# Kernel optimization log

Measured on AMD Instinct MI355X. Metric: run time of the kernel, lower is better.

The kernel has to match this reference:

```python
import jax, jax.numpy as jnp
import numpy as np

D_MODEL = 768
D_STATE = 16
EXPAND = 2
D_INNER = EXPAND * D_MODEL          # 1536
DT_RANK = D_MODEL // 16             # 48 (ceil(d_model/16))
D_CONV = 4
BATCH = 2
SEQ = 1024


def _init_params(key, prefix):
    ks = jax.random.split(key, 6)
    s = 0.02
    p = {}
    p[prefix + '_in_w'] = jax.random.normal(ks[0], (2 * D_INNER, D_MODEL), dtype=jnp.float32) * s
    p[prefix + '_conv_w'] = jax.random.normal(ks[1], (D_INNER, D_CONV), dtype=jnp.float32) * s
    p[prefix + '_conv_b'] = jnp.zeros((D_INNER,), dtype=jnp.float32)
    p[prefix + '_xproj_w'] = jax.random.normal(ks[2], (DT_RANK + 2 * D_STATE, D_INNER), dtype=jnp.float32) * s
    p[prefix + '_dt_w'] = jax.random.normal(ks[3], (D_INNER, DT_RANK), dtype=jnp.float32) * s
    p[prefix + '_dt_b'] = jax.random.normal(ks[4], (D_INNER,), dtype=jnp.float32) * s
    # S4D-real init: A = -[1..d_state] per channel, stored as log
    p[prefix + '_Alog'] = jnp.log(jnp.broadcast_to(jnp.arange(1, D_STATE + 1, dtype=jnp.float32), (D_INNER, D_STATE)))
    p[prefix + '_D'] = jnp.ones((D_INNER,), dtype=jnp.float32)
    p[prefix + '_out_w'] = jax.random.normal(ks[5], (D_MODEL, D_INNER), dtype=jnp.float32) * s
    return p


def setup_inputs() -> dict:
    key = jax.random.key(0)
    kx, kf, kb = jax.random.split(key, 3)
    inp = {'x': jax.random.normal(kx, (BATCH, SEQ, D_MODEL), dtype=jnp.float32)}
    inp.update(_init_params(kf, 'f'))
    inp.update(_init_params(kb, 'b'))
    return inp


def _mamba(x, in_w, conv_w, conv_b, xproj_w, dt_w, dt_b, Alog, Dskip, out_w):
    """One Mamba block (mamba_ssm semantics): in_proj -> causal depthwise conv ->
    SiLU -> (dt, B, C) projections -> selective scan -> SiLU(z) gate -> out_proj."""
    B, L, _ = x.shape
    xz = jnp.einsum('bld,ed->ble', x, in_w)            # (B, L, 2*d_inner)
    u, z = jnp.split(xz, 2, axis=-1)                    # each (B, L, d_inner)
    # causal depthwise conv1d, kernel D_CONV, left pad D_CONV-1
    u_t = u.transpose(0, 2, 1)                          # (B, d_inner, L)
    kern = conv_w[:, None, :]                           # (d_inner, 1, D_CONV)
    u_c = jax.lax.conv_general_dilated(u_t, kern, window_strides=(1,),
                                       padding=[(D_CONV - 1, 0)],
                                       feature_group_count=D_INNER)
    u = jax.nn.silu((u_c + conv_b[None, :, None]).transpose(0, 2, 1))  # (B, L, d_inner)
    x_dbl = jnp.einsum('bld,ed->ble', u, xproj_w)       # (B, L, dt_rank+2*d_state)
    dt, Bm, Cm = jnp.split(x_dbl, [DT_RANK, DT_RANK + D_STATE], axis=-1)
    delta = jax.nn.softplus(jnp.einsum('blr,dr->bld', dt, dt_w) + dt_b)  # (B, L, d_inner)
    A = -jnp.exp(Alog)                                  # (d_inner, d_state)
    dA = jnp.exp(jnp.einsum('bld,dn->bldn', delta, A))  # (B, L, d_inner, d_state)
    dBu = jnp.einsum('bld,bln,bld->bldn', delta, Bm, u) # (B, L, d_inner, d_state)

    def step(h, inp):
        dA_t, dBu_t, C_t = inp                           # (B,d,n),(B,d,n),(B,n)
        h = dA_t * h + dBu_t
        y = jnp.einsum('bdn,bn->bd', h, C_t)
        return h, y

    h0 = jnp.zeros((B, D_INNER, D_STATE), dtype=x.dtype)
    _, ys = jax.lax.scan(step, h0, (dA.transpose(1, 0, 2, 3),
                                    dBu.transpose(1, 0, 2, 3),
                                    Cm.transpose(1, 0, 2)))
    y = ys.transpose(1, 0, 2) + u * Dskip               # (B, L, d_inner)
    y = y * jax.nn.silu(z)
    return jnp.einsum('bld,od->blo', y, out_w)          # (B, L, d_model)


def reference(x, f_in_w, f_conv_w, f_conv_b, f_xproj_w, f_dt_w, f_dt_b, f_Alog, f_D, f_out_w,
              b_in_w, b_conv_w, b_conv_b, b_xproj_w, b_dt_w, b_dt_b, b_Alog, b_D, b_out_w):
    fwd = _mamba(x, f_in_w, f_conv_w, f_conv_b, f_xproj_w, f_dt_w, f_dt_b, f_Alog, f_D, f_out_w)
    bwd = jnp.flip(_mamba(jnp.flip(x, 1), b_in_w, b_conv_w, b_conv_b, b_xproj_w,
                          b_dt_w, b_dt_b, b_Alog, b_D, b_out_w), 1)
    return fwd + bwd  # merge == 'add'
```

## Files before the change

### kernel.cpp

```cpp
#include <hip/hip_runtime.h>

#define BATCH   2
#define SEQ     1024
#define DMODEL  768
#define DINNER  1536
#define DTRANK  48
#define DSTATE  16
#define NROWS   (BATCH*SEQ)
#define NCHUNK  64
#define LCHUNK  16

typedef unsigned short u16;
typedef __attribute__((ext_vector_type(8))) short short8;
typedef __attribute__((ext_vector_type(4))) float floatx4;

#define MFMA16(a,b,c) __builtin_amdgcn_mfma_f32_16x16x32_bf16(a,b,c,0,0,0)

__device__ __forceinline__ float us2f(u16 u) {
    union { unsigned int i; float f; } c; c.i = ((unsigned int)u) << 16; return c.f;
}
__device__ __forceinline__ u16 f2us(float f) {
    union { float f; unsigned int i; } c; c.f = f;
    unsigned int x = c.i;
    unsigned int lsb = (x >> 16) & 1u;
    x += 0x7fffu + lsb;
    return (u16)(x >> 16);
}
__device__ __forceinline__ float softplusf(float x) {
    return (x > 20.f) ? x : log1pf(__expf(x));
}

__device__ __forceinline__ void stage16(const void* g, void* l) {
    __builtin_amdgcn_global_load_lds((const __attribute__((address_space(1))) void*)g,
                                     (__attribute__((address_space(3))) void*)l, 16, 0, 0);
}

__global__ __launch_bounds__(256) void prep_all(
    const float* __restrict__ x,
    const float* __restrict__ fiw, const float* __restrict__ biw,
    const float* __restrict__ fxp, const float* __restrict__ bxp,
    const float* __restrict__ fow, const float* __restrict__ bow,
    const float* __restrict__ fdw, const float* __restrict__ bdw,
    u16* __restrict__ Xb, u16* __restrict__ Wf, u16* __restrict__ Wb,
    u16* __restrict__ XPhf, u16* __restrict__ XPlf,
    u16* __restrict__ XPhb, u16* __restrict__ XPlb,
    u16* __restrict__ Ocf, u16* __restrict__ Ocb,
    u16* __restrict__ DWh, u16* __restrict__ DWl)
{
    const int nx = NROWS * DMODEL;
    const int nw = 2 * DINNER * DMODEL;
    const int np = 128 * DINNER;
    const int no = DMODEL * DINNER;
    const int nd = DINNER * 64;
    int i = blockIdx.x * 256 + threadIdx.x;

    if (i < nx) { Xb[i] = f2us(x[i]); return; }
    i -= nx;
    if (i < nw) { Wf[i] = f2us(fiw[i]); return; }
    i -= nw;
    if (i < nw) { Wb[i] = f2us(biw[i]); return; }
    i -= nw;
    if (i < np) {
        const float f = (i < 80 * DINNER) ? fxp[i] : 0.f;
        const u16 h = f2us(f);
        XPhf[i] = h; XPlf[i] = f2us(f - us2f(h)); return;
    }
    i -= np;
    if (i < np) {
        const float f = (i < 80 * DINNER) ? bxp[i] : 0.f;
        const u16 h = f2us(f);
        XPhb[i] = h; XPlb[i] = f2us(f - us2f(h)); return;
    }
    i -= np;
    if (i < no) { Ocf[i] = f2us(fow[i]); return; }
    i -= no;
    if (i < no) { Ocb[i] = f2us(bow[i]); return; }
    i -= no;
    if (i < nd) {
        const int row = i >> 6, col = i & 63;
        const float f = (col < DTRANK) ? fdw[(size_t)row * DTRANK + col] : 0.f;
        const u16 h = f2us(f);
        DWh[i] = h; DWl[i] = f2us(f - us2f(h)); return;
    }
    i -= nd;
    if (i < nd) {
        const int row = i >> 6, col = i & 63;
        const float f = (col < DTRANK) ? bdw[(size_t)row * DTRANK + col] : 0.f;
        const u16 h = f2us(f);
        DWh[nd + i] = h; DWl[nd + i] = f2us(f - us2f(h));
    }
}

__global__ __launch_bounds__(256) void dprep2(
    const float* __restrict__ PS2,
    u16* __restrict__ XDh, u16* __restrict__ XDl,
    float* __restrict__ xdout)
{
    const int i = blockIdx.x * 256 + threadIdx.x;
    const int n1 = 2 * NROWS * 64;
    if (i < n1) {
        const int row = i >> 6, col = i & 63;
        float f = 0.f;
        if (col < DTRANK) {
            const int dir = row >> 11, r = row & 2047;
#pragma unroll
            for (int k = 0; k < 4; ++k)
                f += PS2[(((size_t)(dir * 4 + k) * NROWS) + r) * 80 + col];
        }
        const u16 h = f2us(f);
        XDh[i] = h;
        XDl[i] = f2us(f - us2f(h));
    } else {
        const int j = i - n1;
        const int row = j >> 5;
        const int col = 48 + (j & 31);
        const int dir = row >> 11, r = row & 2047;
        float f = 0.f;
#pragma unroll
        for (int k = 0; k < 4; ++k)
            f += PS2[(((size_t)(dir * 4 + k) * NROWS) + r) * 80 + col];
        xdout[(size_t)row * 80 + col] = f;
    }
}

__global__ __launch_bounds__(256) void gemm_delta(
    const u16* __restrict__ XDh, const u16* __restrict__ XDl,
    const u16* __restrict__ DWh, const u16* __restrict__ DWl,
    const float* __restrict__ fdtb, const float* __restrict__ bdtb,
    float* __restrict__ DLf, float* __restrict__ DLb)
{
    const int dir = blockIdx.z;
    const u16* ah = XDh + (size_t)dir * NROWS * 64;
    const u16* al = XDl + (size_t)dir * NROWS * 64;
    const u16* bh = DWh + (size_t)dir * DINNER * 64;
    const u16* bl = DWl + (size_t)dir * DINNER * 64;
    const float* bias = dir ? bdtb : fdtb;
    float* C = dir ? DLb : DLf;

    __shared__ __align__(16) u16 sAh[128 * 32];
    __shared__ __align__(16) u16 sAl[128 * 32];
    __shared__ __align__(16) u16 sBh[128 * 32];
    __shared__ __align__(16) u16 sBl[128 * 32];

    const int tid = threadIdx.x;
    const int lane = tid & 63;
    const int wave = tid >> 6;
    const int wm = wave >> 1, wn = wave & 1;
    const int m0 = blockIdx.y * 128, n0 = blockIdx.x * 128;
    const int lm = lane & 15, quad = lane >> 4;

    floatx4 acc[4][4];
#pragma unroll
    for (int i = 0; i < 4; ++i)
#pragma unroll
        for (int j = 0; j < 4; ++j)
            acc[i][j] = (floatx4){0.f, 0.f, 0.f, 0.f};

    for (int kt = 0; kt < 64; kt += 32) {
        __syncthreads();
#pragma unroll
        for (int c = 0; c < 2; ++c) {
            const int seg = wave * 2 + c;
            const int row = seg * 16 + (lane >> 2);
            const int col = kt + (lane & 3) * 8;
            stage16(ah + (size_t)(m0 + row) * 64 + col, (char*)sAh + seg * 1024);
            stage16(al + (size_t)(m0 + row) * 64 + col, (char*)sAl + seg * 1024);
            stage16(bh + (size_t)(n0 + row) * 64 + col, (char*)sBh + seg * 1024);
            stage16(bl + (size_t)(n0 + row) * 64 + col, (char*)sBl + seg * 1024);
        }
        __syncthreads();

        short8 afh[4], afl[4], bfh[4], bfl[4];
#pragma unroll
        for (int i = 0; i < 4; ++i) {
            const int ar = wm * 64 + i * 16 + lm;
            afh[i] = *reinterpret_cast<const short8*>(sAh + ar * 32 + quad * 8);
            afl[i] = *reinterpret_cast<const short8*>(sAl + ar * 32 + quad * 8);
            const int br = wn * 64 + i * 16 + lm;
            bfh[i] = *reinterpret_cast<const short8*>(sBh + br * 32 + quad * 8);
            bfl[i] = *reinterpret_cast<const short8*>(sBl + br * 32 + quad * 8);
        }
#pragma unroll
        for (int i = 0; i < 4; ++i)
#pragma unroll
            for (int j = 0; j < 4; ++j) {
                acc[i][j] = MFMA16(afh[i], bfh[j], acc[i][j]);
                acc[i][j] = MFMA16(afh[i], bfl[j], acc[i][j]);
                acc[i][j] = MFMA16(afl[i], bfh[j], acc[i][j]);
            }
    }

#pragma unroll
    for (int i = 0; i < 4; ++i)
#pragma unroll
        for (int j = 0; j < 4; ++j)
#pragma unroll
            for (int r = 0; r < 4; ++r) {
                const int row = m0 + wm * 64 + i * 16 + quad * 4 + r;
                const int col = n0 + wn * 64 + j * 16 + lm;
                C[(size_t)row * DINNER + col] = softplusf(acc[i][j][r] + bias[col]);
            }
}

__global__ __launch_bounds__(256) void gemm_mfma1(
    const u16* __restrict__ Ab,
    const u16* __restrict__ B0, const u16* __restrict__ B1,
    u16* __restrict__ U0, u16* __restrict__ Z0,
    u16* __restrict__ U1, u16* __restrict__ Z1)
{
    const u16* B = blockIdx.z ? B1 : B0;

    __shared__ __align__(16) u16 sA[128 * 32];
    __shared__ __align__(16) u16 sB[128 * 32];

    const int tid = threadIdx.x;
    const int lane = tid & 63;
    const int wave = tid >> 6;
    const int wm = wave >> 1, wn = wave & 1;
    const int m0 = blockIdx.y * 128, n0 = blockIdx.x * 128;
    const int lm = lane & 15, quad = lane >> 4;

    floatx4 acc[4][4];
#pragma unroll
    for (int i = 0; i < 4; ++i)
#pragma unroll
        for (int j = 0; j < 4; ++j)
            acc[i][j] = (floatx4){0.f, 0.f, 0.f, 0.f};

    for (int kt = 0; kt < DMODEL; kt += 32) {
        __syncthreads();
#pragma unroll
        for (int c = 0; c < 2; ++c) {
            const int seg = wave * 2 + c;
            const int row = seg * 16 + (lane >> 2);
            const int col = kt + (lane & 3) * 8;
            stage16(Ab + (size_t)(m0 + row) * DMODEL + col, (char*)sA + seg * 1024);
            stage16(B + (size_t)(n0 + row) * DMODEL + col, (char*)sB + seg * 1024);
        }
        __syncthreads();

        short8 af[4], bf[4];
#pragma unroll
        for (int i = 0; i < 4; ++i) {
            af[i] = *reinterpret_cast<const short8*>(sA + (wm * 64 + i * 16 + lm) * 32 + quad * 8);
            bf[i] = *reinterpret_cast<const short8*>(sB + (wn * 64 + i * 16 + lm) * 32 + quad * 8);
        }
#pragma unroll
        for (int i = 0; i < 4; ++i)
#pragma unroll
            for (int j = 0; j < 4; ++j)
                acc[i][j] = MFMA16(af[i], bf[j], acc[i][j]);
    }

    const bool isU = (n0 < DINNER);
    u16* dst = blockIdx.z ? (isU ? U1 : Z1) : (isU ? U0 : Z0);
    const int nb = isU ? n0 : n0 - DINNER;
#pragma unroll
    for (int i = 0; i < 4; ++i)
#pragma unroll
        for (int j = 0; j < 4; ++j)
#pragma unroll
            for (int r = 0; r < 4; ++r) {
                const int row = m0 + wm * 64 + i * 16 + quad * 4 + r;
                const int col = nb + wn * 64 + j * 16 + lm;
                dst[(size_t)row * DINNER + col] = f2us(acc[i][j][r]);
            }
}

__global__ __launch_bounds__(256) void gemm_xproj(
    const u16* __restrict__ A0, const u16* __restrict__ A1,
    const u16* __restrict__ Bh0, const u16* __restrict__ Bl0,
    const u16* __restrict__ Bh1, const u16* __restrict__ Bl1,
    float* __restrict__ PS2)
{
    const int dir = blockIdx.y >> 2, kseg = blockIdx.y & 3;
    const u16* A  = dir ? A1 : A0;
    const u16* Bh = dir ? Bh1 : Bh0;
    const u16* Bl = dir ? Bl1 : Bl0;
    float* out = PS2 + (size_t)blockIdx.y * NROWS * 80;

    __shared__ __align__(16) u16 sA[128 * 32];
    __shared__ __align__(16) u16 sBh[128 * 32];
    __shared__ __align__(16) u16 sBl[128 * 32];

    const int tid = threadIdx.x;
    const int lane = tid & 63;
    const int wave = tid >> 6;
    const int wm = wave >> 1, wn = wave & 1;
    const int m0 = blockIdx.x * 128;
    const int lm = lane & 15, quad = lane >> 4;

    floatx4 acc[4][4];
#pragma unroll
    for (int i = 0; i < 4; ++i)
#pragma unroll
        for (int j = 0; j < 4; ++j)
            acc[i][j] = (floatx4){0.f, 0.f, 0.f, 0.f};

    for (int kt = kseg * 384; kt < kseg * 384 + 384; kt += 32) {
        __syncthreads();
#pragma unroll
        for (int c = 0; c < 2; ++c) {
            const int seg = wave * 2 + c;
            const int row = seg * 16 + (lane >> 2);
            const int col = kt + (lane & 3) * 8;
            stage16(A + (size_t)(m0 + row) * DINNER + col, (char*)sA + seg * 1024);
            stage16(Bh + (size_t)row * DINNER + col, (char*)sBh + seg * 1024);
            stage16(Bl + (size_t)row * DINNER + col, (char*)sBl + seg * 1024);
        }
        __syncthreads();

        short8 af[4], bh[4], bl[4];
#pragma unroll
        for (int i = 0; i < 4; ++i) {
            af[i] = *reinterpret_cast<const short8*>(sA + (wm * 64 + i * 16 + lm) * 32 + quad * 8);
            bh[i] = *reinterpret_cast<const short8*>(sBh + (wn * 64 + i * 16 + lm) * 32 + quad * 8);
            bl[i] = *reinterpret_cast<const short8*>(sBl + (wn * 64 + i * 16 + lm) * 32 + quad * 8);
        }
#pragma unroll
        for (int i = 0; i < 4; ++i)
#pragma unroll
            for (int j = 0; j < 4; ++j) {
                acc[i][j] = MFMA16(af[i], bh[j], acc[i][j]);
                acc[i][j] = MFMA16(af[i], bl[j], acc[i][j]);
            }
    }

#pragma unroll
    for (int i = 0; i < 4; ++i)
#pragma unroll
        for (int j = 0; j < 4; ++j)
#pragma unroll
            for (int r = 0; r < 4; ++r) {
                const int row = m0 + wm * 64 + i * 16 + quad * 4 + r;
                const int col = wn * 64 + j * 16 + lm;
                if (col < 80)
                    out[(size_t)row * 80 + col] = acc[i][j][r];
            }
}

__global__ __launch_bounds__(256) void gemm_mfma_out(
    const u16* __restrict__ Y0, const u16* __restrict__ Y1,
    const u16* __restrict__ W0, const u16* __restrict__ W1,
    float* __restrict__ PS)
{
    const int dir = blockIdx.z >> 1, kseg = blockIdx.z & 1;
    const u16* A = dir ? Y1 : Y0;
    const u16* B = dir ? W1 : W0;
    float* out = PS + (size_t)blockIdx.z * NROWS * DMODEL;

    __shared__ __align__(16) u16 sA[128 * 32];
    __shared__ __align__(16) u16 sB[128 * 32];

    const int tid = threadIdx.x;
    const int lane = tid & 63;
    const int wave = tid >> 6;
    const int wm = wave >> 1, wn = wave & 1;
    const int m0 = blockIdx.y * 128, n0 = blockIdx.x * 128;
    const int lm = lane & 15, quad = lane >> 4;

    floatx4 acc[4][4];
#pragma unroll
    for (int i = 0; i < 4; ++i)
#pragma unroll
        for (int j = 0; j < 4; ++j)
            acc[i][j] = (floatx4){0.f, 0.f, 0.f, 0.f};

    for (int kt = kseg * 768; kt < kseg * 768 + 768; kt += 32) {
        __syncthreads();
#pragma unroll
        for (int c = 0; c < 2; ++c) {
            const int seg = wave * 2 + c;
            const int row = seg * 16 + (lane >> 2);
            const int col = kt + (lane & 3) * 8;
            stage16(A + (size_t)(m0 + row) * DINNER + col, (char*)sA + seg * 1024);
            stage16(B + (size_t)(n0 + row) * DINNER + col, (char*)sB + seg * 1024);
        }
        __syncthreads();

        short8 af[4], bf[4];
#pragma unroll
        for (int i = 0; i < 4; ++i) {
            af[i] = *reinterpret_cast<const short8*>(sA + (wm * 64 + i * 16 + lm) * 32 + quad * 8);
            bf[i] = *reinterpret_cast<const short8*>(sB + (wn * 64 + i * 16 + lm) * 32 + quad * 8);
        }
#pragma unroll
        for (int i = 0; i < 4; ++i)
#pragma unroll
            for (int j = 0; j < 4; ++j)
                acc[i][j] = MFMA16(af[i], bf[j], acc[i][j]);
    }

#pragma unroll
    for (int i = 0; i < 4; ++i)
#pragma unroll
        for (int j = 0; j < 4; ++j)
#pragma unroll
            for (int r = 0; r < 4; ++r) {
                const int row = m0 + wm * 64 + i * 16 + quad * 4 + r;
                const int col = n0 + wn * 64 + j * 16 + lm;
                out[(size_t)row * DMODEL + col] = acc[i][j][r];
            }
}

__global__ __launch_bounds__(256) void add4_kernel(
    const float* __restrict__ PS, float* __restrict__ out, int n4)
{
    const int i = blockIdx.x * 256 + threadIdx.x;
    if (i >= n4) return;
    const float4 a = reinterpret_cast<const float4*>(PS)[i];
    const float4 b = reinterpret_cast<const float4*>(PS + (size_t)NROWS * DMODEL)[i];
    const float4 c = reinterpret_cast<const float4*>(PS + (size_t)2 * NROWS * DMODEL)[i];
    const float4 d = reinterpret_cast<const float4*>(PS + (size_t)3 * NROWS * DMODEL)[i];
    reinterpret_cast<float4*>(out)[i] = make_float4(
        (a.x + b.x) + (c.x + d.x), (a.y + b.y) + (c.y + d.y),
        (a.z + b.z) + (c.z + d.z), (a.w + b.w) + (c.w + d.w));
}

__global__ __launch_bounds__(256) void conv_silu8(
    const u16* __restrict__ xuF, const u16* __restrict__ xuB,
    const float* __restrict__ wF, const float* __restrict__ wB,
    const float* __restrict__ bF, const float* __restrict__ bB,
    u16* __restrict__ ucF, u16* __restrict__ ucB)
{
    const int gid = blockIdx.x * 256 + threadIdx.x;
    const int dg = gid % 192;
    const int rest = gid / 192;
    const int bl = rest % NROWS;
    const int dir = rest / NROWS;
    const int b = bl / SEQ, l = bl % SEQ;
    const int d8 = dg * 8;

    const u16* xu   = dir ? xuB : xuF;
    const float* w  = dir ? wB : wF;
    const float* bs = dir ? bB : bF;
    u16* uc         = dir ? ucB : ucF;

    float acc[8];
    {
        const float4 b0 = *reinterpret_cast<const float4*>(bs + d8);
        const float4 b1 = *reinterpret_cast<const float4*>(bs + d8 + 4);
        acc[0]=b0.x; acc[1]=b0.y; acc[2]=b0.z; acc[3]=b0.w;
        acc[4]=b1.x; acc[5]=b1.y; acc[6]=b1.z; acc[7]=b1.w;
    }
    float wk[4][8];
#pragma unroll
    for (int dd = 0; dd < 8; ++dd) {
        const float4 wv = *reinterpret_cast<const float4*>(w + (size_t)(d8 + dd) * 4);
        wk[0][dd]=wv.x; wk[1][dd]=wv.y; wk[2][dd]=wv.z; wk[3][dd]=wv.w;
    }
#pragma unroll
    for (int k = 0; k < 4; ++k) {
        const int ls = (dir == 0) ? (l - 3 + k) : (l + 3 - k);
        if (ls >= 0 && ls < SEQ) {
            const short8 v = *reinterpret_cast<const short8*>(
                xu + ((size_t)b * SEQ + ls) * DINNER + d8);
#pragma unroll
            for (int dd = 0; dd < 8; ++dd)
                acc[dd] = fmaf(wk[k][dd], us2f((u16)v[dd]), acc[dd]);
        }
    }
    u16 out8[8];
#pragma unroll
    for (int dd = 0; dd < 8; ++dd) {
        const float s = acc[dd] * (1.f / (1.f + __expf(-acc[dd])));
        out8[dd] = f2us(s);
    }
    *reinterpret_cast<short8*>(uc + (size_t)bl * DINNER + d8) =
        *reinterpret_cast<const short8*>(out8);
}

__global__ __launch_bounds__(256) void scan_p1(
    const float* __restrict__ dF, const float* __restrict__ dB,
    const u16* __restrict__ ucF, const u16* __restrict__ ucB,
    const float* __restrict__ xdF, const float* __restrict__ xdB,
    float* __restrict__ SMh, float* __restrict__ esPool)
{
    const int bi = blockIdx.x;
    const int c = bi & (NCHUNK - 1);
    const int g = bi / NCHUNK;
    const int dg = g % 6;
    const int b  = (g / 6) & 1;
    const int dir = g / 12;
    const int tid = threadIdx.x;
    const int d = dg * 256 + tid;

    const float* delta = dir ? dB : dF;
    const u16*   uc    = dir ? ucB : ucF;
    const float* xdp   = dir ? xdB : xdF;

    float h[16];
#pragma unroll
    for (int n = 0; n < 16; ++n) h[n] = 0.f;
    float sumD = 0.f;

    for (int t = 0; t < LCHUNK; ++t) {
        const int tt = c * LCHUNK + t;
        const int l = dir ? (SEQ - 1 - tt) : tt;
        const size_t base = (size_t)b * SEQ + l;
        const float dlt = delta[base * DINNER + d];
        const float u   = us2f(uc[base * DINNER + d]);
        const float* xr = xdp + base * 80;
        const float4 B0 = *(const float4*)(xr + 48);
        const float4 B1 = *(const float4*)(xr + 52);
        const float4 B2 = *(const float4*)(xr + 56);
        const float4 B3 = *(const float4*)(xr + 60);
        const float Bv[16] = {B0.x, B0.y, B0.z, B0.w, B1.x, B1.y, B1.z, B1.w,
                              B2.x, B2.y, B2.z, B2.w, B3.x, B3.y, B3.z, B3.w};
        const float du = dlt * u;
        const float e = __expf(-dlt);
        float cur = e;
#pragma unroll
        for (int n = 0; n < 16; ++n) {
            h[n] = fmaf(cur, h[n], du * Bv[n]);
            cur *= e;
        }
        sumD += dlt;
    }
    float4* out = (float4*)(SMh + ((size_t)bi * 256 + tid) * 16);
    out[0] = make_float4(h[0], h[1], h[2], h[3]);
    out[1] = make_float4(h[4], h[5], h[6], h[7]);
    out[2] = make_float4(h[8], h[9], h[10], h[11]);
    out[3] = make_float4(h[12], h[13], h[14], h[15]);
    esPool[bi * 256 + tid] = __expf(-sumD);
}

__global__ __launch_bounds__(256) void scan_mid_par(
    float* __restrict__ SMh, const float* __restrict__ esPool)
{
    const int g = blockIdx.x >> 6;
    const int j = blockIdx.x & 63;
    const int tid = threadIdx.x;
    const int dd = tid >> 6;
    const int c  = tid & 63;
    const int d  = j * 4 + dd;
    const int slot = (g * NCHUNK + c) * 256 + d;

    float4* ph = (float4*)(SMh + (size_t)slot * 16);
    float h[16];
    {
        const float4 a = ph[0], b = ph[1], cc = ph[2], dv = ph[3];
        h[0]=a.x; h[1]=a.y; h[2]=a.z; h[3]=a.w;
        h[4]=b.x; h[5]=b.y; h[6]=b.z; h[7]=b.w;
        h[8]=cc.x; h[9]=cc.y; h[10]=cc.z; h[11]=cc.w;
        h[12]=dv.x; h[13]=dv.y; h[14]=dv.z; h[15]=dv.w;
    }
    float es = esPool[slot];

#pragma unroll
    for (int s = 1; s < NCHUNK; s <<= 1) {
        const float esB = es;
        const float es_p = __shfl_up(es, s, 64);
        float hp[16];
#pragma unroll
        for (int n = 0; n < 16; ++n) hp[n] = __shfl_up(h[n], s, 64);
        if (c >= s) {
            float cur = esB;
#pragma unroll
            for (int n = 0; n < 16; ++n) {
                h[n] = fmaf(cur, hp[n], h[n]);
                cur *= esB;
            }
            es = es_p * esB;
        }
    }
    float hx[16];
#pragma unroll
    for (int n = 0; n < 16; ++n) hx[n] = __shfl_up(h[n], 1, 64);
    if (c == 0) {
#pragma unroll
        for (int n = 0; n < 16; ++n) hx[n] = 0.f;
    }
    ph[0] = make_float4(hx[0], hx[1], hx[2], hx[3]);
    ph[1] = make_float4(hx[4], hx[5], hx[6], hx[7]);
    ph[2] = make_float4(hx[8], hx[9], hx[10], hx[11]);
    ph[3] = make_float4(hx[12], hx[13], hx[14], hx[15]);
}

__global__ __launch_bounds__(256) void scan_p2(
    const float* __restrict__ dF, const float* __restrict__ dB,
    const u16* __restrict__ ucF, const u16* __restrict__ ucB,
    const u16* __restrict__ zF, const u16* __restrict__ zB,
    const float* __restrict__ xdF, const float* __restrict__ xdB,
    const float* __restrict__ DF, const float* __restrict__ DB,
    const float* __restrict__ SMh,
    u16* __restrict__ yF, u16* __restrict__ yB)
{
    const int bi = blockIdx.x;
    const int c = bi & (NCHUNK - 1);
    const int g = bi / NCHUNK;
    const int dg = g % 6;
    const int b  = (g / 6) & 1;
    const int dir = g / 12;
    const int tid = threadIdx.x;
    const int d = dg * 256 + tid;

    const float* delta = dir ? dB : dF;
    const u16*   uc    = dir ? ucB : ucF;
    const u16*   zp    = dir ? zB : zF;
    const float* xdp   = dir ? xdB : xdF;
    u16*         y     = dir ? yB : yF;
    const float  Dd    = (dir ? DB : DF)[d];

    float h[16];
    {
        const float4* ph = (const float4*)(SMh + ((size_t)bi * 256 + tid) * 16);
        const float4 h0 = ph[0], h1 = ph[1], h2 = ph[2], h3 = ph[3];
        h[0]=h0.x; h[1]=h0.y; h[2]=h0.z; h[3]=h0.w;
        h[4]=h1.x; h[5]=h1.y; h[6]=h1.z; h[7]=h1.w;
        h[8]=h2.x; h[9]=h2.y; h[10]=h2.z; h[11]=h2.w;
        h[12]=h3.x; h[13]=h3.y; h[14]=h3.z; h[15]=h3.w;
    }

    for (int t = 0; t < LCHUNK; ++t) {
        const int tt = c * LCHUNK + t;
        const int l = dir ? (SEQ - 1 - tt) : tt;
        const size_t base = (size_t)b * SEQ + l;
        const float dlt = delta[base * DINNER + d];
        const float u   = us2f(uc[base * DINNER + d]);
        const float z   = us2f(zp[base * DINNER + d]);
        const float* xr = xdp + base * 80;
        const float4 B0 = *(const float4*)(xr + 48);
        const float4 B1 = *(const float4*)(xr + 52);
        const float4 B2 = *(const float4*)(xr + 56);
        const float4 B3 = *(const float4*)(xr + 60);
        const float4 C0 = *(const float4*)(xr + 64);
        const float4 C1 = *(const float4*)(xr + 68);
        const float4 C2 = *(const float4*)(xr + 72);
        const float4 C3 = *(const float4*)(xr + 76);
        const float Bv[16] = {B0.x, B0.y, B0.z, B0.w, B1.x, B1.y, B1.z, B1.w,
                              B2.x, B2.y, B2.z, B2.w, B3.x, B3.y, B3.z, B3.w};
        const float Cv[16] = {C0.x, C0.y, C0.z, C0.w, C1.x, C1.y, C1.z, C1.w,
                              C2.x, C2.y, C2.z, C2.w, C3.x, C3.y, C3.z, C3.w};
        const float du = dlt * u;
        const float e = __expf(-dlt);
        float cur = e;
        float yv = 0.f;
#pragma unroll
        for (int n = 0; n < 16; ++n) {
            h[n] = fmaf(cur, h[n], du * Bv[n]);
            yv = fmaf(h[n], Cv[n], yv);
            cur *= e;
        }
        yv += u * Dd;
        yv *= z * (1.f / (1.f + __expf(-z)));
        y[base * DINNER + d] = f2us(yv);
    }
}

extern "C" void kernel_launch(void* const* d_in, const int* in_sizes, int n_in,
                              void* d_out, int out_size, void* d_ws, size_t ws_size,
                              hipStream_t stream) {
    const float* x        = (const float*)d_in[0];
    const float* f_in_w   = (const float*)d_in[1];
    const float* f_conv_w = (const float*)d_in[2];
    const float* f_conv_b = (const float*)d_in[3];
    const float* f_xproj  = (const float*)d_in[4];
    const float* f_dt_w   = (const float*)d_in[5];
    const float* f_dt_b   = (const float*)d_in[6];
    const float* f_D      = (const float*)d_in[8];
    const float* f_out_w  = (const float*)d_in[9];
    const float* b_in_w   = (const float*)d_in[10];
    const float* b_conv_w = (const float*)d_in[11];
    const float* b_conv_b = (const float*)d_in[12];
    const float* b_xproj  = (const float*)d_in[13];
    const float* b_dt_w   = (const float*)d_in[14];
    const float* b_dt_b   = (const float*)d_in[15];
    const float* b_D      = (const float*)d_in[17];
    const float* b_out_w  = (const float*)d_in[18];

    char* ws = (char*)d_ws;
    size_t off = 0;
    auto carve = [&](size_t bytes) { char* p = ws + off; off += (bytes + 255) & ~(size_t)255; return p; };
    u16*   XU   = (u16*)  carve(2 * (size_t)NROWS * DINNER * 2);
    u16*   XZz  = (u16*)  carve(2 * (size_t)NROWS * DINNER * 2);
    u16*   UC   = (u16*)  carve(2 * (size_t)NROWS * DINNER * 2);
    u16*   Y    = (u16*)  carve(2 * (size_t)NROWS * DINNER * 2);
    float* XD   = (float*)carve(2 * (size_t)NROWS * 80 * 4);
    float* DL   = (float*)carve(2 * (size_t)NROWS * DINNER * 4);
    u16*   Xb   = (u16*)  carve((size_t)NROWS * DMODEL * 2);
    u16*   Wf   = (u16*)  carve(2 * (size_t)DINNER * DMODEL * 2);
    u16*   Wb   = (u16*)  carve(2 * (size_t)DINNER * DMODEL * 2);
    u16*   XPhf = (u16*)  carve(128 * (size_t)DINNER * 2);
    u16*   XPlf = (u16*)  carve(128 * (size_t)DINNER * 2);
    u16*   XPhb = (u16*)  carve(128 * (size_t)DINNER * 2);
    u16*   XPlb = (u16*)  carve(128 * (size_t)DINNER * 2);
    u16*   Ocf  = (u16*)  carve((size_t)DMODEL * DINNER * 2);
    u16*   Ocb  = (u16*)  carve((size_t)DMODEL * DINNER * 2);
    u16*   DWh  = (u16*)  carve(2 * (size_t)DINNER * 64 * 2);
    u16*   DWl  = (u16*)  carve(2 * (size_t)DINNER * 64 * 2);
    u16*   XDh  = (u16*)  carve(2 * (size_t)NROWS * 64 * 2);
    u16*   XDl  = (u16*)  carve(2 * (size_t)NROWS * 64 * 2);
    float* PS2  = (float*)carve(8 * (size_t)NROWS * 80 * 4);
    float* SMh  = (float*)carve((size_t)24 * NCHUNK * 256 * 16 * 4);
    float* esPool = (float*)carve((size_t)24 * NCHUNK * 256 * 4);
    float* PS   = (float*)carve(4 * (size_t)NROWS * DMODEL * 4);

    u16* XUb  = XU  + (size_t)NROWS * DINNER;
    u16* XZzb = XZz + (size_t)NROWS * DINNER;
    u16* UCb  = UC  + (size_t)NROWS * DINNER;
    u16* Yb   = Y   + (size_t)NROWS * DINNER;
    float* XDb = XD + (size_t)NROWS * 80;
    float* DLb = DL + (size_t)NROWS * DINNER;

    const dim3 blk(256);
    const int nprep = NROWS * DMODEL + 2 * (2 * DINNER * DMODEL) + 2 * (128 * DINNER)
                    + 2 * (DMODEL * DINNER) + 2 * (DINNER * 64);

    prep_all<<<dim3((nprep + 255) / 256), blk, 0, stream>>>(
        x, f_in_w, b_in_w, f_xproj, b_xproj, f_out_w, b_out_w, f_dt_w, b_dt_w,
        Xb, Wf, Wb, XPhf, XPlf, XPhb, XPlb, Ocf, Ocb, DWh, DWl);

    gemm_mfma1<<<dim3(2 * DINNER / 128, NROWS / 128, 2), blk, 0, stream>>>(
        Xb, Wf, Wb, XU, XZz, XUb, XZzb);

    conv_silu8<<<dim3(2 * NROWS * 192 / 256), blk, 0, stream>>>(
        XU, XUb, f_conv_w, b_conv_w, f_conv_b, b_conv_b, UC, UCb);

    gemm_xproj<<<dim3(NROWS / 128, 8), blk, 0, stream>>>(
        UC, UCb, XPhf, XPlf, XPhb, XPlb, PS2);

    dprep2<<<dim3((2 * NROWS * 64 + 2 * NROWS * 32) / 256), blk, 0, stream>>>(
        PS2, XDh, XDl, XD);

    gemm_delta<<<dim3(DINNER / 128, NROWS / 128, 2), blk, 0, stream>>>(
        XDh, XDl, DWh, DWl, f_dt_b, b_dt_b, DL, DLb);

    scan_p1<<<dim3(24 * NCHUNK), blk, 0, stream>>>(
        DL, DLb, UC, UCb, XD, XDb, SMh, esPool);

    scan_mid_par<<<dim3(24 * 64), blk, 0, stream>>>(SMh, esPool);

    scan_p2<<<dim3(24 * NCHUNK), blk, 0, stream>>>(
        DL, DLb, UC, UCb, XZz, XZzb, XD, XDb,
        f_D, b_D, SMh, Y, Yb);

    gemm_mfma_out<<<dim3(DMODEL / 128, NROWS / 128, 4), blk, 0, stream>>>(
        Y, Yb, Ocf, Ocb, PS);

    add4_kernel<<<dim3((NROWS * DMODEL / 4 + 255) / 256), blk, 0, stream>>>(
        PS, (float*)d_out, NROWS * DMODEL / 4);
}
```

Measured before the change: 314.4 us.

## Replace split-bf16 delta GEMM with fused fp32 VALU kernel and enlarge scan chunks

Removes the dprep2 split-precision conversion pass and the three-MFMA bf16 hi/lo delta GEMM. In their place, one fp32 VALU kernel reduces the partial x_proj sums into shared memory, keeps the 48 dt weights per channel in registers, and writes softplus(delta) directly. It also halves the number of scan chunks (chunk length 16 to 32) and adapts the chunk-prefix kernel to 32-wide shuffles. This saves a launch and intermediate traffic but puts the delta projection on scalar FMAs, and the longer chunks lengthen the sequential part of each scan pass.

```diff
diff --git a/kernel.cpp b/kernel.cpp
--- a/kernel.cpp
+++ b/kernel.cpp
@@ -7,8 +7,8 @@
 #define DTRANK  48
 #define DSTATE  16
 #define NROWS   (BATCH*SEQ)
-#define NCHUNK  64
-#define LCHUNK  16
+#define NCHUNK  32
+#define LCHUNK  32
 
 typedef unsigned short u16;
 typedef __attribute__((ext_vector_type(8))) short short8;
@@ -45,13 +45,13 @@
     u16* __restrict__ XPhf, u16* __restrict__ XPlf,
     u16* __restrict__ XPhb, u16* __restrict__ XPlb,
     u16* __restrict__ Ocf, u16* __restrict__ Ocb,
-    u16* __restrict__ DWh, u16* __restrict__ DWl)
+    float* __restrict__ DWT)
 {
     const int nx = NROWS * DMODEL;
     const int nw = 2 * DINNER * DMODEL;
     const int np = 128 * DINNER;
     const int no = DMODEL * DINNER;
-    const int nd = DINNER * 64;
+    const int nt = 2 * DTRANK * DINNER;
     int i = blockIdx.x * 256 + threadIdx.x;
 
     if (i < nx) { Xb[i] = f2us(x[i]); return; }
@@ -76,130 +76,71 @@
     i -= no;
     if (i < no) { Ocb[i] = f2us(bow[i]); return; }
     i -= no;
-    if (i < nd) {
-        const int row = i >> 6, col = i & 63;
-        const float f = (col < DTRANK) ? fdw[(size_t)row * DTRANK + col] : 0.f;
-        const u16 h = f2us(f);
-        DWh[i] = h; DWl[i] = f2us(f - us2f(h)); return;
-    }
-    i -= nd;
-    if (i < nd) {
-        const int row = i >> 6, col = i & 63;
-        const float f = (col < DTRANK) ? bdw[(size_t)row * DTRANK + col] : 0.f;
-        const u16 h = f2us(f);
-        DWh[nd + i] = h; DWl[nd + i] = f2us(f - us2f(h));
-    }
-}
-
-__global__ __launch_bounds__(256) void dprep2(
-    const float* __restrict__ PS2,
-    u16* __restrict__ XDh, u16* __restrict__ XDl,
-    float* __restrict__ xdout)
-{
-    const int i = blockIdx.x * 256 + threadIdx.x;
-    const int n1 = 2 * NROWS * 64;
-    if (i < n1) {
-        const int row = i >> 6, col = i & 63;
+    if (i < nt) {
+        const int dir = i / (DTRANK * DINNER);
+        const int rem = i % (DTRANK * DINNER);
+        const int k = rem / DINNER, d = rem % DINNER;
+        const float* w = dir ? bdw : fdw;
+        DWT[i] = w[(size_t)d * DTRANK + k];
+    }
+}
+
+__global__ __launch_bounds__(256) void delta_valu(
+    const float* __restrict__ PS2, const float* __restrict__ DWT,
+    const float* __restrict__ fdtb, const float* __restrict__ bdtb,
+    float* __restrict__ xdout,
+    float* __restrict__ DLf, float* __restrict__ DLb)
+{
+    const int slab = blockIdx.x / 6;
+    const int dg   = blockIdx.x % 6;
+    const int r0   = slab * 64;
+    const int dir  = r0 >> 11;
+    const int tid  = threadIdx.x;
+    const int d    = dg * 256 + tid;
+
+    __shared__ float sxd[64][48];
+
+    for (int j = tid; j < 64 * 48; j += 256) {
+        const int rr = r0 + j / 48;
+        const int col = j % 48;
+        const int rl = rr & 2047;
         float f = 0.f;
-        if (col < DTRANK) {
-            const int dir = row >> 11, r = row & 2047;
+#pragma unroll
+        for (int k = 0; k < 4; ++k)
+            f += PS2[(((size_t)(dir * 4 + k) * NROWS) + rl) * 80 + col];
+        sxd[j / 48][col] = f;
+    }
+    if (dg == 0) {
+        for (int j = tid; j < 64 * 32; j += 256) {
+            const int rr = r0 + j / 32;
+            const int col = 48 + (j % 32);
+            const int rl = rr & 2047;
+            float f = 0.f;
 #pragma unroll
             for (int k = 0; k < 4; ++k)
-                f += PS2[(((size_t)(dir * 4 + k) * NROWS) + r) * 80 + col];
-        }
-        const u16 h = f2us(f);
-        XDh[i] = h;
-        XDl[i] = f2us(f - us2f(h));
-    } else {
-        const int j = i - n1;
-        const int row = j >> 5;
-        const int col = 48 + (j & 31);
-        const int dir = row >> 11, r = row & 2047;
-        float f = 0.f;
-#pragma unroll
-        for (int k = 0; k < 4; ++k)
-            f += PS2[(((size_t)(dir * 4 + k) * NROWS) + r) * 80 + col];
-        xdout[(size_t)row * 80 + col] = f;
-    }
-}
-
-__global__ __launch_bounds__(256) void gemm_delta(
-    const u16* __restrict__ XDh, const u16* __restrict__ XDl,
-    const u16* __restrict__ DWh, const u16* __restrict__ DWl,
-    const float* __restrict__ fdtb, const float* __restrict__ bdtb,
-    float* __restrict__ DLf, float* __restrict__ DLb)
-{
-    const int dir = blockIdx.z;
-    const u16* ah = XDh + (size_t)dir * NROWS * 64;
-    const u16* al = XDl + (size_t)dir * NROWS * 64;
-    const u16* bh = DWh + (size_t)dir * DINNER * 64;
-    const u16* bl = DWl + (size_t)dir * DINNER * 64;
-    const float* bias = dir ? bdtb : fdtb;
-    float* C = dir ? DLb : DLf;
-
-    __shared__ __align__(16) u16 sAh[128 * 32];
-    __shared__ __align__(16) u16 sAl[128 * 32];
-    __shared__ __align__(16) u16 sBh[128 * 32];
-    __shared__ __align__(16) u16 sBl[128 * 32];
-
-    const int tid = threadIdx.x;
-    const int lane = tid & 63;
-    const int wave = tid >> 6;
-    const int wm = wave >> 1, wn = wave & 1;
-    const int m0 = blockIdx.y * 128, n0 = blockIdx.x * 128;
-    const int lm = lane & 15, quad = lane >> 4;
-
-    floatx4 acc[4][4];
-#pragma unroll
-    for (int i = 0; i < 4; ++i)
-#pragma unroll
-        for (int j = 0; j < 4; ++j)
-            acc[i][j] = (floatx4){0.f, 0.f, 0.f, 0.f};
-
-    for (int kt = 0; kt < 64; kt += 32) {
-        __syncthreads();
-#pragma unroll
-        for (int c = 0; c < 2; ++c) {
-            const int seg = wave * 2 + c;
-            const int row = seg * 16 + (lane >> 2);
-            const int col = kt + (lane & 3) * 8;
-            stage16(ah + (size_t)(m0 + row) * 64 + col, (char*)sAh + seg * 1024);
-            stage16(al + (size_t)(m0 + row) * 64 + col, (char*)sAl + seg * 1024);
-            stage16(bh + (size_t)(n0 + row) * 64 + col, (char*)sBh + seg * 1024);
-            stage16(bl + (size_t)(n0 + row) * 64 + col, (char*)sBl + seg * 1024);
-        }
-        __syncthreads();
-
-        short8 afh[4], afl[4], bfh[4], bfl[4];
-#pragma unroll
-        for (int i = 0; i < 4; ++i) {
-            const int ar = wm * 64 + i * 16 + lm;
-            afh[i] = *reinterpret_cast<const short8*>(sAh + ar * 32 + quad * 8);
-            afl[i] = *reinterpret_cast<const short8*>(sAl + ar * 32 + quad * 8);
-            const int br = wn * 64 + i * 16 + lm;
-            bfh[i] = *reinterpret_cast<const short8*>(sBh + br * 32 + quad * 8);
-            bfl[i] = *reinterpret_cast<const short8*>(sBl + br * 32 + quad * 8);
-        }
-#pragma unroll
-        for (int i = 0; i < 4; ++i)
-#pragma unroll
-            for (int j = 0; j < 4; ++j) {
-                acc[i][j] = MFMA16(afh[i], bfh[j], acc[i][j]);
-                acc[i][j] = MFMA16(afh[i], bfl[j], acc[i][j]);
-                acc[i][j] = MFMA16(afl[i], bfh[j], acc[i][j]);
-            }
-    }
-
-#pragma unroll
-    for (int i = 0; i < 4; ++i)
-#pragma unroll
-        for (int j = 0; j < 4; ++j)
-#pragma unroll
-            for (int r = 0; r < 4; ++r) {
-                const int row = m0 + wm * 64 + i * 16 + quad * 4 + r;
-                const int col = n0 + wn * 64 + j * 16 + lm;
-                C[(size_t)row * DINNER + col] = softplusf(acc[i][j][r] + bias[col]);
-            }
+                f += PS2[(((size_t)(dir * 4 + k) * NROWS) + rl) * 80 + col];
+            xdout[(size_t)rr * 80 + col] = f;
+        }
+    }
+
+    float dw[48];
+    {
+        const float* wt = DWT + (size_t)dir * DTRANK * DINNER;
+#pragma unroll
+        for (int k = 0; k < 48; ++k) dw[k] = wt[(size_t)k * DINNER + d];
+    }
+    const float dtb = (dir ? bdtb : fdtb)[d];
+    float* DL = dir ? DLb : DLf;
+    __syncthreads();
+
+    for (int rr = 0; rr < 64; ++rr) {
+        float acc = dtb;
+#pragma unroll
+        for (int k = 0; k < 48; ++k)
+            acc = fmaf(sxd[rr][k], dw[k], acc);
+        const int rl = (r0 + rr) & 2047;
+        DL[(size_t)rl * DINNER + d] = softplusf(acc);
+    }
 }
 
 __global__ __launch_bounds__(256) void gemm_mfma1(
@@ -528,12 +469,12 @@
 __global__ __launch_bounds__(256) void scan_mid_par(
     float* __restrict__ SMh, const float* __restrict__ esPool)
 {
-    const int g = blockIdx.x >> 6;
-    const int j = blockIdx.x & 63;
+    const int g = blockIdx.x >> 5;
+    const int j = blockIdx.x & 31;
     const int tid = threadIdx.x;
-    const int dd = tid >> 6;
-    const int c  = tid & 63;
-    const int d  = j * 4 + dd;
+    const int dd = tid >> 5;
+    const int c  = tid & 31;
+    const int d  = j * 8 + dd;
     const int slot = (g * NCHUNK + c) * 256 + d;
 
     float4* ph = (float4*)(SMh + (size_t)slot * 16);
@@ -550,10 +491,10 @@
 #pragma unroll
     for (int s = 1; s < NCHUNK; s <<= 1) {
         const float esB = es;
-        const float es_p = __shfl_up(es, s, 64);
+        const float es_p = __shfl_up(es, s, 32);
         float hp[16];
 #pragma unroll
-        for (int n = 0; n < 16; ++n) hp[n] = __shfl_up(h[n], s, 64);
+        for (int n = 0; n < 16; ++n) hp[n] = __shfl_up(h[n], s, 32);
         if (c >= s) {
             float cur = esB;
 #pragma unroll
@@ -566,7 +507,7 @@
     }
     float hx[16];
 #pragma unroll
-    for (int n = 0; n < 16; ++n) hx[n] = __shfl_up(h[n], 1, 64);
+    for (int n = 0; n < 16; ++n) hx[n] = __shfl_up(h[n], 1, 32);
     if (c == 0) {
 #pragma unroll
         for (int n = 0; n < 16; ++n) hx[n] = 0.f;
@@ -687,10 +628,7 @@
     u16*   XPlb = (u16*)  carve(128 * (size_t)DINNER * 2);
     u16*   Ocf  = (u16*)  carve((size_t)DMODEL * DINNER * 2);
     u16*   Ocb  = (u16*)  carve((size_t)DMODEL * DINNER * 2);
-    u16*   DWh  = (u16*)  carve(2 * (size_t)DINNER * 64 * 2);
-    u16*   DWl  = (u16*)  carve(2 * (size_t)DINNER * 64 * 2);
-    u16*   XDh  = (u16*)  carve(2 * (size_t)NROWS * 64 * 2);
-    u16*   XDl  = (u16*)  carve(2 * (size_t)NROWS * 64 * 2);
+    float* DWT  = (float*)carve(2 * (size_t)DTRANK * DINNER * 4);
     float* PS2  = (float*)carve(8 * (size_t)NROWS * 80 * 4);
     float* SMh  = (float*)carve((size_t)24 * NCHUNK * 256 * 16 * 4);
     float* esPool = (float*)carve((size_t)24 * NCHUNK * 256 * 4);
@@ -705,11 +643,11 @@
 
     const dim3 blk(256);
     const int nprep = NROWS * DMODEL + 2 * (2 * DINNER * DMODEL) + 2 * (128 * DINNER)
-                    + 2 * (DMODEL * DINNER) + 2 * (DINNER * 64);
+                    + 2 * (DMODEL * DINNER) + 2 * (DTRANK * DINNER);
 
     prep_all<<<dim3((nprep + 255) / 256), blk, 0, stream>>>(
         x, f_in_w, b_in_w, f_xproj, b_xproj, f_out_w, b_out_w, f_dt_w, b_dt_w,
-        Xb, Wf, Wb, XPhf, XPlf, XPhb, XPlb, Ocf, Ocb, DWh, DWl);
+        Xb, Wf, Wb, XPhf, XPlf, XPhb, XPlb, Ocf, Ocb, DWT);
 
     gemm_mfma1<<<dim3(2 * DINNER / 128, NROWS / 128, 2), blk, 0, stream>>>(
         Xb, Wf, Wb, XU, XZz, XUb, XZzb);
@@ -720,16 +658,13 @@
     gemm_xproj<<<dim3(NROWS / 128, 8), blk, 0, stream>>>(
         UC, UCb, XPhf, XPlf, XPhb, XPlb, PS2);
 
-    dprep2<<<dim3((2 * NROWS * 64 + 2 * NROWS * 32) / 256), blk, 0, stream>>>(
-        PS2, XDh, XDl, XD);
-
-    gemm_delta<<<dim3(DINNER / 128, NROWS / 128, 2), blk, 0, stream>>>(
-        XDh, XDl, DWh, DWl, f_dt_b, b_dt_b, DL, DLb);
+    delta_valu<<<dim3(64 * 6), blk, 0, stream>>>(
+        PS2, DWT, f_dt_b, b_dt_b, XD, DL, DLb);
 
     scan_p1<<<dim3(24 * NCHUNK), blk, 0, stream>>>(
         DL, DLb, UC, UCb, XD, XDb, SMh, esPool);
 
-    scan_mid_par<<<dim3(24 * 64), blk, 0, stream>>>(SMh, esPool);
+    scan_mid_par<<<dim3(24 * 32), blk, 0, stream>>>(SMh, esPool);
 
     scan_p2<<<dim3(24 * NCHUNK), blk, 0, stream>>>(
         DL, DLb, UC, UCb, XZz, XZzb, XD, XDb,
```

Measured after the change: 317.8 us. Within noise of the previous version (+1.1%).

## Fuse three-phase chunked scan into one cooperative kernel with grid syncs

Applied to the files above, without the earlier changes.

Merges scan_p1, scan_mid_par and scan_p2 into a single cooperative kernel that uses grid.sync() between the chunk-local scan, the cross-chunk prefix combine and the output pass. The chunk count is halved to 32 chunks of 32 steps so that 768 blocks can be co-resident for a cooperative launch, and the mid-phase shuffle width is reduced to 32. The goal is to remove two kernel launches and their gaps. In exchange each block runs a longer serial recurrence, there is less parallelism, and the two grid barriers add cost.

```diff
diff --git a/kernel.cpp b/kernel.cpp
--- a/kernel.cpp
+++ b/kernel.cpp
@@ -1,4 +1,5 @@
 #include <hip/hip_runtime.h>
+#include <hip/hip_cooperative_groups.h>
 
 #define BATCH   2
 #define SEQ     1024
@@ -7,8 +8,8 @@
 #define DTRANK  48
 #define DSTATE  16
 #define NROWS   (BATCH*SEQ)
-#define NCHUNK  64
-#define LCHUNK  16
+#define NCHUNK  32
+#define LCHUNK  32
 
 typedef unsigned short u16;
 typedef __attribute__((ext_vector_type(8))) short short8;
@@ -470,12 +471,17 @@
         *reinterpret_cast<const short8*>(out8);
 }
 
-__global__ __launch_bounds__(256) void scan_p1(
+__global__ __launch_bounds__(256) void scan_fused(
     const float* __restrict__ dF, const float* __restrict__ dB,
     const u16* __restrict__ ucF, const u16* __restrict__ ucB,
+    const u16* __restrict__ zF, const u16* __restrict__ zB,
     const float* __restrict__ xdF, const float* __restrict__ xdB,
-    float* __restrict__ SMh, float* __restrict__ esPool)
-{
+    const float* __restrict__ DF, const float* __restrict__ DB,
+    float* __restrict__ SMh, float* __restrict__ esPool,
+    u16* __restrict__ yF, u16* __restrict__ yB)
+{
+    cooperative_groups::grid_group grid = cooperative_groups::this_grid();
+
     const int bi = blockIdx.x;
     const int c = bi & (NCHUNK - 1);
     const int g = bi / NCHUNK;
@@ -487,7 +493,10 @@
 
     const float* delta = dir ? dB : dF;
     const u16*   uc    = dir ? ucB : ucF;
+    const u16*   zp    = dir ? zB : zF;
     const float* xdp   = dir ? xdB : xdF;
+    u16*         y     = dir ? yB : yF;
+    const float  Dd    = (dir ? DB : DF)[d];
 
     float h[16];
 #pragma unroll
@@ -517,92 +526,68 @@
         }
         sumD += dlt;
     }
-    float4* out = (float4*)(SMh + ((size_t)bi * 256 + tid) * 16);
-    out[0] = make_float4(h[0], h[1], h[2], h[3]);
-    out[1] = make_float4(h[4], h[5], h[6], h[7]);
-    out[2] = make_float4(h[8], h[9], h[10], h[11]);
-    out[3] = make_float4(h[12], h[13], h[14], h[15]);
-    esPool[bi * 256 + tid] = __expf(-sumD);
-}
-
-__global__ __launch_bounds__(256) void scan_mid_par(
-    float* __restrict__ SMh, const float* __restrict__ esPool)
-{
-    const int g = blockIdx.x >> 6;
-    const int j = blockIdx.x & 63;
-    const int tid = threadIdx.x;
-    const int dd = tid >> 6;
-    const int c  = tid & 63;
-    const int d  = j * 4 + dd;
-    const int slot = (g * NCHUNK + c) * 256 + d;
-
-    float4* ph = (float4*)(SMh + (size_t)slot * 16);
-    float h[16];
     {
-        const float4 a = ph[0], b = ph[1], cc = ph[2], dv = ph[3];
-        h[0]=a.x; h[1]=a.y; h[2]=a.z; h[3]=a.w;
-        h[4]=b.x; h[5]=b.y; h[6]=b.z; h[7]=b.w;
-        h[8]=cc.x; h[9]=cc.y; h[10]=cc.z; h[11]=cc.w;
-        h[12]=dv.x; h[13]=dv.y; h[14]=dv.z; h[15]=dv.w;
-    }
-    float es = esPool[slot];
-
-#pragma unroll
-    for (int s = 1; s < NCHUNK; s <<= 1) {
-        const float esB = es;
-        const float es_p = __shfl_up(es, s, 64);
-        float hp[16];
-#pragma unroll
-        for (int n = 0; n < 16; ++n) hp[n] = __shfl_up(h[n], s, 64);
-        if (c >= s) {
-            float cur = esB;
-#pragma unroll
-            for (int n = 0; n < 16; ++n) {
-                h[n] = fmaf(cur, hp[n], h[n]);
-                cur *= esB;
+        float4* out = (float4*)(SMh + ((size_t)bi * 256 + tid) * 16);
+        out[0] = make_float4(h[0], h[1], h[2], h[3]);
+        out[1] = make_float4(h[4], h[5], h[6], h[7]);
+        out[2] = make_float4(h[8], h[9], h[10], h[11]);
+        out[3] = make_float4(h[12], h[13], h[14], h[15]);
+        esPool[bi * 256 + tid] = __expf(-sumD);
+    }
+
+    grid.sync();
+
+    {
+        const int g2 = blockIdx.x >> 5;
+        const int j  = blockIdx.x & 31;
+        const int dd = tid >> 5;
+        const int cc = tid & 31;
+        const int d2 = j * 8 + dd;
+        const int slot = (g2 * NCHUNK + cc) * 256 + d2;
+
+        float4* ph = (float4*)(SMh + (size_t)slot * 16);
+        float hh[16];
+        {
+            const float4 a = ph[0], bb = ph[1], c2 = ph[2], dv = ph[3];
+            hh[0]=a.x; hh[1]=a.y; hh[2]=a.z; hh[3]=a.w;
+            hh[4]=bb.x; hh[5]=bb.y; hh[6]=bb.z; hh[7]=bb.w;
+            hh[8]=c2.x; hh[9]=c2.y; hh[10]=c2.z; hh[11]=c2.w;
+            hh[12]=dv.x; hh[13]=dv.y; hh[14]=dv.z; hh[15]=dv.w;
+        }
+        float es = esPool[slot];
+
+#pragma unroll
+        for (int s = 1; s < NCHUNK; s <<= 1) {
+            const float esB = es;
+            const float es_p = __shfl_up(es, s, 32);
+            float hp[16];
+#pragma unroll
+            for (int n = 0; n < 16; ++n) hp[n] = __shfl_up(hh[n], s, 32);
+            if (cc >= s) {
+                float cur = esB;
+#pragma unroll
+                for (int n = 0; n < 16; ++n) {
+                    hh[n] = fmaf(cur, hp[n], hh[n]);
+                    cur *= esB;
+                }
+                es = es_p * esB;
             }
-            es = es_p * esB;
-        }
-    }
-    float hx[16];
-#pragma unroll
-    for (int n = 0; n < 16; ++n) hx[n] = __shfl_up(h[n], 1, 64);
-    if (c == 0) {
-#pragma unroll
-        for (int n = 0; n < 16; ++n) hx[n] = 0.f;
-    }
-    ph[0] = make_float4(hx[0], hx[1], hx[2], hx[3]);
-    ph[1] = make_float4(hx[4], hx[5], hx[6], hx[7]);
-    ph[2] = make_float4(hx[8], hx[9], hx[10], hx[11]);
-    ph[3] = make_float4(hx[12], hx[13], hx[14], hx[15]);
-}
-
-__global__ __launch_bounds__(256) void scan_p2(
-    const float* __restrict__ dF, const float* __restrict__ dB,
-    const u16* __restrict__ ucF, const u16* __restrict__ ucB,
-    const u16* __restrict__ zF, const u16* __restrict__ zB,
-    const float* __restrict__ xdF, const float* __restrict__ xdB,
-    const float* __restrict__ DF, const float* __restrict__ DB,
-    const float* __restrict__ SMh,
-    u16* __restrict__ yF, u16* __restrict__ yB)
-{
-    const int bi = blockIdx.x;
-    const int c = bi & (NCHUNK - 1);
-    const int g = bi / NCHUNK;
-    const int dg = g % 6;
-    const int b  = (g / 6) & 1;
-    const int dir = g / 12;
-    const int tid = threadIdx.x;
-    const int d = dg * 256 + tid;
-
-    const float* delta = dir ? dB : dF;
-    const u16*   uc    = dir ? ucB : ucF;
-    const u16*   zp    = dir ? zB : zF;
-    const float* xdp   = dir ? xdB : xdF;
-    u16*         y     = dir ? yB : yF;
-    const float  Dd    = (dir ? DB : DF)[d];
-
-    float h[16];
+        }
+        float hx[16];
+#pragma unroll
+        for (int n = 0; n < 16; ++n) hx[n] = __shfl_up(hh[n], 1, 32);
+        if (cc == 0) {
+#pragma unroll
+            for (int n = 0; n < 16; ++n) hx[n] = 0.f;
+        }
+        ph[0] = make_float4(hx[0], hx[1], hx[2], hx[3]);
+        ph[1] = make_float4(hx[4], hx[5], hx[6], hx[7]);
+        ph[2] = make_float4(hx[8], hx[9], hx[10], hx[11]);
+        ph[3] = make_float4(hx[12], hx[13], hx[14], hx[15]);
+    }
+
+    grid.sync();
+
     {
         const float4* ph = (const float4*)(SMh + ((size_t)bi * 256 + tid) * 16);
         const float4 h0 = ph[0], h1 = ph[1], h2 = ph[2], h3 = ph[3];
@@ -726,14 +711,16 @@
     gemm_delta<<<dim3(DINNER / 128, NROWS / 128, 2), blk, 0, stream>>>(
         XDh, XDl, DWh, DWl, f_dt_b, b_dt_b, DL, DLb);
 
-    scan_p1<<<dim3(24 * NCHUNK), blk, 0, stream>>>(
-        DL, DLb, UC, UCb, XD, XDb, SMh, esPool);
-
-    scan_mid_par<<<dim3(24 * 64), blk, 0, stream>>>(SMh, esPool);
-
-    scan_p2<<<dim3(24 * NCHUNK), blk, 0, stream>>>(
-        DL, DLb, UC, UCb, XZz, XZzb, XD, XDb,
-        f_D, b_D, SMh, Y, Yb);
+    {
+        void* args[] = {
+            (void*)&DL, (void*)&DLb, (void*)&UC, (void*)&UCb,
+            (void*)&XZz, (void*)&XZzb, (void*)&XD, (void*)&XDb,
+            (void*)&f_D, (void*)&b_D, (void*)&SMh, (void*)&esPool,
+            (void*)&Y, (void*)&Yb
+        };
+        hipLaunchCooperativeKernel((void*)scan_fused, dim3(24 * NCHUNK), blk,
+                                   args, 0, stream);
+    }
 
     gemm_mfma_out<<<dim3(DMODEL / 128, NROWS / 128, 4), blk, 0, stream>>>(
         Y, Yb, Ocf, Ocb, PS);
```

New measurement: 534.4 us. 1.7x slower.
